# Optimization experiments

Hardware: AMD Instinct MI355X
Metric: run time of the kernel (lower is better)

The kernel has to match this reference:

```python
import jax, jax.numpy as jnp
import numpy as np

N = 100000      # nodes
E = 1600000     # edges
F_IN = 128      # in_feat
H = 128         # hidden_dim
C = 40          # num_class


def setup_inputs() -> dict:
    key = jax.random.key(0)
    ks = jax.random.split(key, 4)
    x = jax.random.normal(ks[0], (N, F_IN), dtype=jnp.float32)
    edge_index = jax.random.randint(ks[1], (2, E), 0, N, dtype=jnp.int32)
    # glorot-ish init for the two GCN layers
    W1 = jax.random.normal(ks[2], (F_IN, H), dtype=jnp.float32) * (1.0 / np.sqrt(F_IN))
    b1 = jnp.zeros((H,), dtype=jnp.float32)
    W2 = jax.random.normal(ks[3], (H, C), dtype=jnp.float32) * (1.0 / np.sqrt(H))
    b2 = jnp.zeros((C,), dtype=jnp.float32)
    return {"x": x, "edge_index": edge_index, "W1": W1, "b1": b1, "W2": W2, "b2": b2}


def _gcn_conv(x, W, b, row, col, norm, n_nodes):
    # GCNConv: linear transform, then normalized sum-aggregation over edges, + bias
    h = x @ W                                  # [N, d_out]
    msg = h[row] * norm[:, None]               # gather sources, scale  [E', d_out]
    out = jax.ops.segment_sum(msg, col, num_segments=n_nodes)  # scatter-add to targets
    return out + b


def reference(x, edge_index, W1, b1, W2, b2):
    n_nodes = x.shape[0]
    # add self-loops (PyG GCNConv default)
    loops = jnp.arange(n_nodes, dtype=edge_index.dtype)
    row = jnp.concatenate([edge_index[0], loops])  # sources
    col = jnp.concatenate([edge_index[1], loops])  # targets
    # symmetric normalization: deg computed at targets with unit edge weights
    deg = jax.ops.segment_sum(jnp.ones_like(col, dtype=x.dtype), col, num_segments=n_nodes)
    dis = jnp.where(deg > 0, jax.lax.rsqrt(jnp.maximum(deg, 1e-12)), 0.0)
    norm = dis[row] * dis[col]                 # [E+N]

    h = jax.nn.relu(_gcn_conv(x, W1, b1, row, col, norm, n_nodes))
    out = _gcn_conv(h, W2, b2, row, col, norm, n_nodes)
    return out
```

## Files before the change

kernel.cpp:

```cpp
#include <hip/hip_runtime.h>
#include <hip/hip_bf16.h>


#define FB_SHIFT 9
#define SLAB_SHIFT 14

__device__ __forceinline__ unsigned bf16rn(float f) {
    unsigned x = __float_as_uint(f);
    unsigned r = ((x >> 16) & 1u) + 0x7fffu;
    return (x + r) >> 16;
}
__device__ __forceinline__ float bf_lo(unsigned u) { return __uint_as_float(u << 16); }
__device__ __forceinline__ float bf_hi(unsigned u) { return __uint_as_float(u & 0xffff0000u); }

typedef __bf16 bf16x8 __attribute__((ext_vector_type(8)));
typedef float  f32x4  __attribute__((ext_vector_type(4)));

__global__ __launch_bounds__(512) void k_binfill(const int* __restrict__ row,
                                                 const int* __restrict__ col,
                                                 int* __restrict__ bcur,
                                                 unsigned* __restrict__ bins, int E,
                                                 int nEB,
                                                 const float* __restrict__ W1,
                                                 const float* __restrict__ W2,
                                                 unsigned* __restrict__ Wt,
                                                 unsigned* __restrict__ W2t) {
    const int tid = threadIdx.x;

    if (blockIdx.x >= nEB) {
        int w = (blockIdx.x - nEB) * 512 + tid;
        if (w < 8192) {
            int n = w >> 6, kk = (w & 63) * 2;
            unsigned lo = bf16rn(W1[(size_t)kk * 128 + n]);
            unsigned hi = bf16rn(W1[(size_t)(kk + 1) * 128 + n]);
            Wt[w] = lo | (hi << 16);
        } else if (w < 8192 + 3072) {
            int u = w - 8192;
            int n = u >> 6, kk = (u & 63) * 2;
            unsigned lo = 0, hi = 0;
            if (n < 40) {
                lo = bf16rn(W2[(size_t)kk * 40 + n]);
                hi = bf16rn(W2[(size_t)(kk + 1) * 40 + n]);
            }
            W2t[u] = lo | (hi << 16);
        }
        return;
    }

    __shared__ int hist[256];
    __shared__ int scn[256];
    __shared__ int gbase[256];
    __shared__ int rcnt[256];
    __shared__ unsigned stage[4096];
    __shared__ unsigned char bkts[4096];

    const int base = blockIdx.x * 4096;

    if (tid < 256) { hist[tid] = 0; rcnt[tid] = 0; }
    __syncthreads();

    unsigned mypk[8];
    int      myb[8];
#pragma unroll
    for (int k = 0; k < 8; ++k) {
        int e = base + k * 512 + tid;
        if (e < E) {
            int r = row[e], c = col[e];
            int b = c >> FB_SHIFT;
            mypk[k] = ((unsigned)r << FB_SHIFT) | (unsigned)(c & ((1 << FB_SHIFT) - 1));
            myb[k] = b;
            atomicAdd(&hist[b], 1);
        } else {
            myb[k] = -1;
        }
    }
    __syncthreads();

    int v = 0;
    if (tid < 256) { v = hist[tid]; scn[tid] = v; }
    __syncthreads();
#pragma unroll
    for (int off = 1; off < 256; off <<= 1) {
        int t = (tid >= off && tid < 256) ? scn[tid - off] : 0;
        __syncthreads();
        if (tid < 256) scn[tid] += t;
        __syncthreads();
    }
    if (tid < 256) {
        int excl = scn[tid] - v;
        scn[tid] = excl;
    }
    __syncthreads();

#pragma unroll
    for (int k = 0; k < 8; ++k) {
        int b = myb[k];
        if (b >= 0) {
            int slot = scn[b] + atomicAdd(&rcnt[b], 1);
            stage[slot] = mypk[k];
            bkts[slot] = (unsigned char)b;
        }
    }

    if (tid < 256 && hist[tid] > 0) gbase[tid] = atomicAdd(&bcur[tid], hist[tid]);
    __syncthreads();

    int total = scn[255] + hist[255];
    const int cap = 1 << SLAB_SHIFT;
    for (int s = tid; s < total; s += 512) {
        unsigned u = stage[s];
        int b = bkts[s];
        int off = gbase[b] + (s - scn[b]);
        if (off < cap)
            bins[((size_t)b << SLAB_SHIFT) + off] = u;
    }
}

__global__ __launch_bounds__(1024) void k_fill2(const unsigned* __restrict__ bins,
                                                const int* __restrict__ bcur,
                                                int2* __restrict__ rpse,
                                                float* __restrict__ dis,
                                                int* __restrict__ pair, int N) {
    __shared__ int cnt[512];
    __shared__ int lcur[512];
    __shared__ int ssum[256];
    const int tid = threadIdx.x;
    const int b = blockIdx.x;
    const int n0 = b << FB_SHIFT;
    const int start = b << SLAB_SHIFT;
    int count = bcur[b];
    if (count > (1 << SLAB_SHIFT)) count = 1 << SLAB_SHIFT;
    const int end = start + count;

    if (tid < 512) cnt[tid] = 0;
    __syncthreads();

    for (int i = start + tid; i < end; i += 1024)
        atomicAdd(&cnt[bins[i] & ((1 << FB_SHIFT) - 1)], 1);
    __syncthreads();

    int c0 = 0, c1 = 0, vsum = 0;
    if (tid < 256) {
        c0 = cnt[2 * tid]; c1 = cnt[2 * tid + 1];
        vsum = c0 + c1;
        ssum[tid] = vsum;
    }
    __syncthreads();
#pragma unroll
    for (int off = 1; off < 256; off <<= 1) {
        int u = (tid >= off && tid < 256) ? ssum[tid - off] : 0;
        __syncthreads();
        if (tid < 256) ssum[tid] += u;
        __syncthreads();
    }
    if (tid < 256) {
        int e0 = start + ssum[tid] - vsum;
        int e1 = e0 + c0;
        lcur[2 * tid] = e0;
        lcur[2 * tid + 1] = e1;
        int node0 = n0 + 2 * tid;
        int node1 = node0 + 1;
        if (node0 < N) {
            rpse[node0] = make_int2(e0, e1);
            dis[node0] = rsqrtf((float)(c0 + 1));
        }
        if (node1 < N) {
            rpse[node1] = make_int2(e1, e1 + c1);
            dis[node1] = rsqrtf((float)(c1 + 1));
        }
    }
    __syncthreads();

    for (int i = start + tid; i < end; i += 1024) {
        unsigned u = bins[i];
        int pos = atomicAdd(&lcur[u & ((1 << FB_SHIFT) - 1)], 1);
        pair[pos] = (int)(u >> FB_SHIFT);
    }
}

__global__ __launch_bounds__(256) void k_cvtx(const float* __restrict__ x,
                                              const float* __restrict__ dis,
                                              unsigned* __restrict__ xb, int n32) {
    int i = blockIdx.x * 256 + threadIdx.x;
    if (i >= n32) return;
    float4 v = ((const float4*)x)[i];
    float d = dis[i >> 5];
    uint2 o;
    o.x = bf16rn(v.x * d) | (bf16rn(v.y * d) << 16);
    o.y = bf16rn(v.z * d) | (bf16rn(v.w * d) << 16);
    ((uint2*)xb)[i] = o;
}

__global__ __launch_bounds__(256) void k_gather1(const unsigned* __restrict__ xb,
                                                 const int2* __restrict__ rpse,
                                                 const int* __restrict__ pair,
                                                 const float* __restrict__ dis,
                                                 unsigned* __restrict__ xab, int N) {
    int gw = (blockIdx.x * 256 + threadIdx.x) >> 6;
    int lane = threadIdx.x & 63;
    if (gw >= N) return;
    float dv = dis[gw];
    unsigned us = xb[(size_t)gw * 64 + lane];
    float2 acc = make_float2(bf_lo(us), bf_hi(us));
    int2 rp = rpse[gw];
    int j = rp.x, je = rp.y;

    for (; j + 7 < je; j += 8) {
        int r0 = pair[j],     r1 = pair[j + 1], r2 = pair[j + 2], r3 = pair[j + 3];
        int r4 = pair[j + 4], r5 = pair[j + 5], r6 = pair[j + 6], r7 = pair[j + 7];
        unsigned a0 = xb[(size_t)r0 * 64 + lane];
        unsigned a1 = xb[(size_t)r1 * 64 + lane];
        unsigned a2 = xb[(size_t)r2 * 64 + lane];
        unsigned a3 = xb[(size_t)r3 * 64 + lane];
        unsigned a4 = xb[(size_t)r4 * 64 + lane];
        unsigned a5 = xb[(size_t)r5 * 64 + lane];
        unsigned a6 = xb[(size_t)r6 * 64 + lane];
        unsigned a7 = xb[(size_t)r7 * 64 + lane];
        acc.x += bf_lo(a0); acc.y += bf_hi(a0);
        acc.x += bf_lo(a1); acc.y += bf_hi(a1);
        acc.x += bf_lo(a2); acc.y += bf_hi(a2);
        acc.x += bf_lo(a3); acc.y += bf_hi(a3);
        acc.x += bf_lo(a4); acc.y += bf_hi(a4);
        acc.x += bf_lo(a5); acc.y += bf_hi(a5);
        acc.x += bf_lo(a6); acc.y += bf_hi(a6);
        acc.x += bf_lo(a7); acc.y += bf_hi(a7);
    }
    for (; j + 3 < je; j += 4) {
        int r0 = pair[j], r1 = pair[j + 1], r2 = pair[j + 2], r3 = pair[j + 3];
        unsigned a0 = xb[(size_t)r0 * 64 + lane];
        unsigned a1 = xb[(size_t)r1 * 64 + lane];
        unsigned a2 = xb[(size_t)r2 * 64 + lane];
        unsigned a3 = xb[(size_t)r3 * 64 + lane];
        acc.x += bf_lo(a0); acc.y += bf_hi(a0);
        acc.x += bf_lo(a1); acc.y += bf_hi(a1);
        acc.x += bf_lo(a2); acc.y += bf_hi(a2);
        acc.x += bf_lo(a3); acc.y += bf_hi(a3);
    }
    for (; j < je; ++j) {
        unsigned a0 = xb[(size_t)pair[j] * 64 + lane];
        acc.x += bf_lo(a0); acc.y += bf_hi(a0);
    }
    xab[(size_t)gw * 64 + lane] = bf16rn(dv * acc.x) | (bf16rn(dv * acc.y) << 16);
}

__global__ __launch_bounds__(256) void k_gemm12(const unsigned* __restrict__ Ab,
                                                const unsigned* __restrict__ Wt,
                                                const unsigned* __restrict__ W2t,
                                                const float* __restrict__ bias,
                                                const float* __restrict__ dis,
                                                unsigned* __restrict__ Zb, int M) {
    __shared__ char smem[70144];
    char* Abase = smem;
    char* Bbase = smem + 34816;
    float* ldis = (float*)(smem + 69632);

    const int tid = threadIdx.x;
    const int r0 = blockIdx.x * 128;

#pragma unroll
    for (int s = 0; s < 8; ++s) {
        int l = tid + s * 256;
        int row = l >> 4, q = l & 15;
        uint4 va = *(const uint4*)(Ab + (size_t)(r0 + row) * 64 + q * 4);
        *(uint4*)(Abase + row * 272 + q * 16) = va;
        uint4 vb = *(const uint4*)(Wt + (size_t)row * 64 + q * 4);
        *(uint4*)(Bbase + row * 272 + q * 16) = vb;
    }
    if (tid < 128) {
        int rr = r0 + tid;
        ldis[tid] = (rr < M) ? dis[rr] : 0.f;
    }
    __syncthreads();

    const int wv = tid >> 6, lane = tid & 63;
    const int quad = lane >> 4, mcol = lane & 15;

    f32x4 acc1[2][8];
#pragma unroll
    for (int rt = 0; rt < 2; ++rt)
#pragma unroll
        for (int ct = 0; ct < 8; ++ct) acc1[rt][ct] = (f32x4){0.f, 0.f, 0.f, 0.f};

#pragma unroll
    for (int ks = 0; ks < 4; ++ks) {
        bf16x8 a[2], b[8];
#pragma unroll
        for (int rt = 0; rt < 2; ++rt) {
            int row = wv * 32 + rt * 16 + mcol;
            a[rt] = *(const bf16x8*)(Abase + row * 272 + ks * 64 + quad * 16);
        }
#pragma unroll
        for (int ct = 0; ct < 8; ++ct) {
            int n = ct * 16 + mcol;
            b[ct] = *(const bf16x8*)(Bbase + n * 272 + ks * 64 + quad * 16);
        }
#pragma unroll
        for (int rt = 0; rt < 2; ++rt)
#pragma unroll
            for (int ct = 0; ct < 8; ++ct)
                acc1[rt][ct] = __builtin_amdgcn_mfma_f32_16x16x32_bf16(
                    a[rt], b[ct], acc1[rt][ct], 0, 0, 0);
    }
    __syncthreads();

    unsigned short* Hs = (unsigned short*)Bbase;
#pragma unroll
    for (int rt = 0; rt < 2; ++rt)
#pragma unroll
        for (int ct = 0; ct < 8; ++ct) {
            float bb = bias[ct * 16 + mcol];
#pragma unroll
            for (int r = 0; r < 4; ++r) {
                float v = acc1[rt][ct][r] + bb;
                v = v > 0.f ? v : 0.f;
                int orow = wv * 32 + rt * 16 + quad * 4 + r;
                Hs[orow * 136 + ct * 16 + mcol] = (unsigned short)bf16rn(v);
            }
        }
#pragma unroll
    for (int s = 0; s < 3; ++s) {
        int l = tid + s * 256;
        int row = l >> 4, q = l & 15;
        uint4 vb = *(const uint4*)(W2t + (size_t)row * 64 + q * 4);
        *(uint4*)(Abase + row * 272 + q * 16) = vb;
    }
    __syncthreads();

    f32x4 acc2[2][3];
#pragma unroll
    for (int rt = 0; rt < 2; ++rt)
#pragma unroll
        for (int ct = 0; ct < 3; ++ct) acc2[rt][ct] = (f32x4){0.f, 0.f, 0.f, 0.f};

#pragma unroll
    for (int ks = 0; ks < 4; ++ks) {
        bf16x8 a[2], b[3];
#pragma unroll
        for (int rt = 0; rt < 2; ++rt) {
            int row = wv * 32 + rt * 16 + mcol;
            a[rt] = *(const bf16x8*)(Bbase + row * 272 + ks * 64 + quad * 16);
        }
#pragma unroll
        for (int ct = 0; ct < 3; ++ct) {
            int n = ct * 16 + mcol;
            b[ct] = *(const bf16x8*)(Abase + n * 272 + ks * 64 + quad * 16);
        }
#pragma unroll
        for (int rt = 0; rt < 2; ++rt)
#pragma unroll
            for (int ct = 0; ct < 3; ++ct)
                acc2[rt][ct] = __builtin_amdgcn_mfma_f32_16x16x32_bf16(
                    a[rt], b[ct], acc2[rt][ct], 0, 0, 0);
    }
    __syncthreads();

    unsigned short* Zs = (unsigned short*)(Abase + 16384);
#pragma unroll
    for (int rt = 0; rt < 2; ++rt)
#pragma unroll
        for (int ct = 0; ct < 3; ++ct) {
#pragma unroll
            for (int r = 0; r < 4; ++r) {
                int orow = wv * 32 + rt * 16 + quad * 4 + r;
                float v = acc2[rt][ct][r] * ldis[orow];
                Zs[orow * 56 + ct * 16 + mcol] = (unsigned short)bf16rn(v);
            }
        }
    __syncthreads();

    if (tid < 128) {
        int rr = r0 + tid;
        if (rr < M) {
            const uint4* s4 = (const uint4*)(Abase + 16384 + tid * 112);
            uint4* d4 = (uint4*)(Zb + ((size_t)rr << 5));
#pragma unroll
            for (int q = 0; q < 5; ++q) d4[q] = s4[q];
        }
    }
}

__global__ __launch_bounds__(256) void k_gather2(const unsigned* __restrict__ zb,
                                                 const int2* __restrict__ rpse,
                                                 const int* __restrict__ pair,
                                                 const float* __restrict__ dis,
                                                 const float* __restrict__ b2,
                                                 float* __restrict__ out, int N) {
    int gw = (blockIdx.x * 256 + threadIdx.x) >> 6;
    int lane = threadIdx.x & 63;
    if (gw >= N) return;
    int sub = lane >> 5;
    int sl  = lane & 31;
    int f   = (sl < 20) ? sl : 19;

    float2 acc = make_float2(0.f, 0.f);
    float dv = dis[gw];
    if (sub == 0) {
        unsigned u = zb[((size_t)gw << 5) + f];
        acc.x = bf_lo(u); acc.y = bf_hi(u);
    }

    int2 rp = rpse[gw];
    int j = rp.x, je = rp.y;
    for (; j + 15 < je; j += 16) {
        int rA = pair[j + sub];
        int rB = pair[j + 2 + sub];
        int rC = pair[j + 4 + sub];
        int rD = pair[j + 6 + sub];
        int rE = pair[j + 8 + sub];
        int rF = pair[j + 10 + sub];
        int rG = pair[j + 12 + sub];
        int rH = pair[j + 14 + sub];
        unsigned uA = zb[((size_t)rA << 5) + f];
        unsigned uB = zb[((size_t)rB << 5) + f];
        unsigned uC = zb[((size_t)rC << 5) + f];
        unsigned uD = zb[((size_t)rD << 5) + f];
        unsigned uE = zb[((size_t)rE << 5) + f];
        unsigned uF = zb[((size_t)rF << 5) + f];
        unsigned uG = zb[((size_t)rG << 5) + f];
        unsigned uH = zb[((size_t)rH << 5) + f];
        acc.x += bf_lo(uA); acc.y += bf_hi(uA);
        acc.x += bf_lo(uB); acc.y += bf_hi(uB);
        acc.x += bf_lo(uC); acc.y += bf_hi(uC);
        acc.x += bf_lo(uD); acc.y += bf_hi(uD);
        acc.x += bf_lo(uE); acc.y += bf_hi(uE);
        acc.x += bf_lo(uF); acc.y += bf_hi(uF);
        acc.x += bf_lo(uG); acc.y += bf_hi(uG);
        acc.x += bf_lo(uH); acc.y += bf_hi(uH);
    }
    for (; j + 7 < je; j += 8) {
        int rA = pair[j + sub];
        int rB = pair[j + 2 + sub];
        int rC = pair[j + 4 + sub];
        int rD = pair[j + 6 + sub];
        unsigned uA = zb[((size_t)rA << 5) + f];
        unsigned uB = zb[((size_t)rB << 5) + f];
        unsigned uC = zb[((size_t)rC << 5) + f];
        unsigned uD = zb[((size_t)rD << 5) + f];
        acc.x += bf_lo(uA); acc.y += bf_hi(uA);
        acc.x += bf_lo(uB); acc.y += bf_hi(uB);
        acc.x += bf_lo(uC); acc.y += bf_hi(uC);
        acc.x += bf_lo(uD); acc.y += bf_hi(uD);
    }
    for (; j + 3 < je; j += 4) {
        int rA = pair[j + sub];
        int rB = pair[j + 2 + sub];
        unsigned uA = zb[((size_t)rA << 5) + f];
        unsigned uB = zb[((size_t)rB << 5) + f];
        acc.x += bf_lo(uA); acc.y += bf_hi(uA);
        acc.x += bf_lo(uB); acc.y += bf_hi(uB);
    }
    for (; j + 1 < je; j += 2) {
        unsigned u = zb[((size_t)pair[j + sub] << 5) + f];
        acc.x += bf_lo(u); acc.y += bf_hi(u);
    }
    if (j < je && sub == 0) {
        unsigned u = zb[((size_t)pair[j] << 5) + f];
        acc.x += bf_lo(u); acc.y += bf_hi(u);
    }

    float bx = __shfl(acc.x, sl + 32, 64);
    float by = __shfl(acc.y, sl + 32, 64);
    if (sub == 0 && sl < 20) {
        float2 bias = ((const float2*)b2)[sl];
        float2 res = make_float2((acc.x + bx) * dv + bias.x,
                                 (acc.y + by) * dv + bias.y);
        ((float2*)(out + (size_t)gw * 40))[sl] = res;
    }
}

extern "C" void kernel_launch(void* const* d_in, const int* in_sizes, int n_in,
                              void* d_out, int out_size, void* d_ws, size_t ws_size,
                              hipStream_t stream) {
    const float* x  = (const float*)d_in[0];
    const int*   ei = (const int*)d_in[1];
    const float* W1 = (const float*)d_in[2];
    const float* b1 = (const float*)d_in[3];
    const float* W2 = (const float*)d_in[4];
    const float* b2 = (const float*)d_in[5];
    float* out = (float*)d_out;

    const int N = in_sizes[0] / 128;
    const int E = in_sizes[1] / 2;
    const int* row = ei;
    const int* col = ei + E;

    const int Np = (N + 255) & ~255;
    const int nbuck = (N + (1 << FB_SHIFT) - 1) >> FB_SHIFT;
    const int nEB = (E + 4095) / 4096;

    int*      bcur   = (int*)d_ws;
    int2*     rpse   = (int2*)(bcur + 256);
    float*    dis    = (float*)(rpse + Np);
    unsigned* Wt     = (unsigned*)(dis + Np);
    unsigned* W2t    = Wt + 8192;
    int*      pair   = (int*)(W2t + 3072);
    unsigned* xb     = (unsigned*)(pair + ((size_t)256 << SLAB_SHIFT));
    unsigned* xab    = xb + (size_t)N * 64;
    unsigned* zb     = xab + (size_t)N * 64;
    unsigned* bins   = (unsigned*)xab;

    hipMemsetAsync(bcur, 0, 256 * sizeof(int), stream);
    k_binfill<<<nEB + 22, 512, 0, stream>>>(row, col, bcur, bins, E, nEB,
                                            W1, W2, Wt, W2t);
    k_fill2<<<nbuck, 1024, 0, stream>>>(bins, bcur, rpse, dis, pair, N);

    k_cvtx<<<(N * 32 + 255) / 256, 256, 0, stream>>>(x, dis, xb, N * 32);

    k_gather1<<<(N + 3) / 4, 256, 0, stream>>>(xb, rpse, pair, dis, xab, N);

    k_gemm12<<<(N + 127) / 128, 256, 0, stream>>>(xab, Wt, W2t, b1, dis, zb, N);

    k_gather2<<<(N + 3) / 4, 256, 0, stream>>>(zb, rpse, pair, dis, b2, out, N);
}
```

Baseline: 261.6 us.

## Slice features into 8 slabs and gather one slab per block, 8 edges per wave

The bf16 scaled features are stored as 8 column slabs of 16 features (32 bytes per node). The layer-1 gather launches one block per slab per 4 nodes, and each wave splits into 8 edge groups of 8 lanes. The groups work on separate edges in parallel and are combined with cross-lane shuffles. The goal is to keep each slab's working set small enough to stay in cache and to get more edges in flight per wave, at the cost of smaller 32-byte random reads, 8x more blocks, re-reading the edge index list once per slab, and the shuffle reduction.

```diff
diff --git a/kernel.cpp b/kernel.cpp
--- a/kernel.cpp
+++ b/kernel.cpp
@@ -180,67 +180,77 @@
 
 __global__ __launch_bounds__(256) void k_cvtx(const float* __restrict__ x,
                                               const float* __restrict__ dis,
-                                              unsigned* __restrict__ xb, int n32) {
+                                              unsigned* __restrict__ xbs, int N) {
     int i = blockIdx.x * 256 + threadIdx.x;
-    if (i >= n32) return;
+    if (i >= N * 32) return;
+    int n = i >> 5;
+    int k2 = (i & 31) * 2;
     float4 v = ((const float4*)x)[i];
-    float d = dis[i >> 5];
+    float d = dis[n];
     uint2 o;
     o.x = bf16rn(v.x * d) | (bf16rn(v.y * d) << 16);
     o.y = bf16rn(v.z * d) | (bf16rn(v.w * d) << 16);
-    ((uint2*)xb)[i] = o;
-}
-
-__global__ __launch_bounds__(256) void k_gather1(const unsigned* __restrict__ xb,
-                                                 const int2* __restrict__ rpse,
-                                                 const int* __restrict__ pair,
-                                                 const float* __restrict__ dis,
-                                                 unsigned* __restrict__ xab, int N) {
-    int gw = (blockIdx.x * 256 + threadIdx.x) >> 6;
-    int lane = threadIdx.x & 63;
+    int s = k2 >> 3, f = k2 & 7;
+    *(uint2*)(xbs + ((size_t)s * N + n) * 8 + f) = o;
+}
+
+__global__ __launch_bounds__(256) void k_gather1s(const unsigned* __restrict__ xbs,
+                                                  const int2* __restrict__ rpse,
+                                                  const int* __restrict__ pair,
+                                                  const float* __restrict__ dis,
+                                                  unsigned* __restrict__ xab, int N) {
+    const int bid = blockIdx.x;
+    const int s = bid & 7;
+    const int wv = threadIdx.x >> 6;
+    const int gw = (bid >> 3) * 4 + wv;
     if (gw >= N) return;
-    float dv = dis[gw];
-    unsigned us = xb[(size_t)gw * 64 + lane];
-    float2 acc = make_float2(bf_lo(us), bf_hi(us));
+    const int lane = threadIdx.x & 63;
+    const int eg = lane >> 3;
+    const int fl = lane & 7;
+
+    const unsigned* base = xbs + (size_t)s * N * 8;
+
+    float ax = 0.f, ay = 0.f;
+    if (eg == 0) {
+        unsigned u = base[(size_t)gw * 8 + fl];
+        ax = bf_lo(u); ay = bf_hi(u);
+    }
+
     int2 rp = rpse[gw];
-    int j = rp.x, je = rp.y;
-
+    int j = rp.x;
+    const int je = rp.y;
+
+    for (; j + 15 < je; j += 16) {
+        int r0 = pair[j + eg];
+        int r1 = pair[j + 8 + eg];
+        unsigned u0 = base[(size_t)r0 * 8 + fl];
+        unsigned u1 = base[(size_t)r1 * 8 + fl];
+        ax += bf_lo(u0); ay += bf_hi(u0);
+        ax += bf_lo(u1); ay += bf_hi(u1);
+    }
     for (; j + 7 < je; j += 8) {
-        int r0 = pair[j],     r1 = pair[j + 1], r2 = pair[j + 2], r3 = pair[j + 3];
-        int r4 = pair[j + 4], r5 = pair[j + 5], r6 = pair[j + 6], r7 = pair[j + 7];
-        unsigned a0 = xb[(size_t)r0 * 64 + lane];
-        unsigned a1 = xb[(size_t)r1 * 64 + lane];
-        unsigned a2 = xb[(size_t)r2 * 64 + lane];
-        unsigned a3 = xb[(size_t)r3 * 64 + lane];
-        unsigned a4 = xb[(size_t)r4 * 64 + lane];
-        unsigned a5 = xb[(size_t)r5 * 64 + lane];
-        unsigned a6 = xb[(size_t)r6 * 64 + lane];
-        unsigned a7 = xb[(size_t)r7 * 64 + lane];
-        acc.x += bf_lo(a0); acc.y += bf_hi(a0);
-        acc.x += bf_lo(a1); acc.y += bf_hi(a1);
-        acc.x += bf_lo(a2); acc.y += bf_hi(a2);
-        acc.x += bf_lo(a3); acc.y += bf_hi(a3);
-        acc.x += bf_lo(a4); acc.y += bf_hi(a4);
-        acc.x += bf_lo(a5); acc.y += bf_hi(a5);
-        acc.x += bf_lo(a6); acc.y += bf_hi(a6);
-        acc.x += bf_lo(a7); acc.y += bf_hi(a7);
-    }
-    for (; j + 3 < je; j += 4) {
-        int r0 = pair[j], r1 = pair[j + 1], r2 = pair[j + 2], r3 = pair[j + 3];
-        unsigned a0 = xb[(size_t)r0 * 64 + lane];
-        unsigned a1 = xb[(size_t)r1 * 64 + lane];
-        unsigned a2 = xb[(size_t)r2 * 64 + lane];
-        unsigned a3 = xb[(size_t)r3 * 64 + lane];
-        acc.x += bf_lo(a0); acc.y += bf_hi(a0);
-        acc.x += bf_lo(a1); acc.y += bf_hi(a1);
-        acc.x += bf_lo(a2); acc.y += bf_hi(a2);
-        acc.x += bf_lo(a3); acc.y += bf_hi(a3);
-    }
-    for (; j < je; ++j) {
-        unsigned a0 = xb[(size_t)pair[j] * 64 + lane];
-        acc.x += bf_lo(a0); acc.y += bf_hi(a0);
-    }
-    xab[(size_t)gw * 64 + lane] = bf16rn(dv * acc.x) | (bf16rn(dv * acc.y) << 16);
+        int r0 = pair[j + eg];
+        unsigned u0 = base[(size_t)r0 * 8 + fl];
+        ax += bf_lo(u0); ay += bf_hi(u0);
+    }
+    if (j + eg < je) {
+        int r0 = pair[j + eg];
+        unsigned u0 = base[(size_t)r0 * 8 + fl];
+        ax += bf_lo(u0); ay += bf_hi(u0);
+    }
+
+    ax += __shfl_xor(ax, 8, 64);
+    ay += __shfl_xor(ay, 8, 64);
+    ax += __shfl_xor(ax, 16, 64);
+    ay += __shfl_xor(ay, 16, 64);
+    ax += __shfl_xor(ax, 32, 64);
+    ay += __shfl_xor(ay, 32, 64);
+
+    if (eg == 0) {
+        float dv = dis[gw];
+        xab[(size_t)gw * 64 + s * 8 + fl] =
+            bf16rn(dv * ax) | (bf16rn(dv * ay) << 16);
+    }
 }
 
 __global__ __launch_bounds__(256) void k_gemm12(const unsigned* __restrict__ Ab,
@@ -494,8 +504,8 @@
     unsigned* Wt     = (unsigned*)(dis + Np);
     unsigned* W2t    = Wt + 8192;
     int*      pair   = (int*)(W2t + 3072);
-    unsigned* xb     = (unsigned*)(pair + ((size_t)256 << SLAB_SHIFT));
-    unsigned* xab    = xb + (size_t)N * 64;
+    unsigned* xbs    = (unsigned*)(pair + ((size_t)256 << SLAB_SHIFT));
+    unsigned* xab    = xbs + (size_t)N * 64;
     unsigned* zb     = xab + (size_t)N * 64;
     unsigned* bins   = (unsigned*)xab;
 
@@ -504,9 +514,9 @@
                                             W1, W2, Wt, W2t);
     k_fill2<<<nbuck, 1024, 0, stream>>>(bins, bcur, rpse, dis, pair, N);
 
-    k_cvtx<<<(N * 32 + 255) / 256, 256, 0, stream>>>(x, dis, xb, N * 32);
-
-    k_gather1<<<(N + 3) / 4, 256, 0, stream>>>(xb, rpse, pair, dis, xab, N);
+    k_cvtx<<<(N * 32 + 255) / 256, 256, 0, stream>>>(x, dis, xbs, N);
+
+    k_gather1s<<<((N + 3) / 4) * 8, 256, 0, stream>>>(xbs, rpse, pair, dis, xab, N);
 
     k_gemm12<<<(N + 127) / 128, 256, 0, stream>>>(xab, Wt, W2t, b1, dis, zb, N);
 
```

Measured after the change: 438.6 us. 67.7% more time.
